# Kernel optimization log

Measured on AMD Instinct MI355X. Metric: run time of the kernel, lower is better.

## Reference

```python
import jax, jax.numpy as jnp
import numpy as np
import math

B, S, D, H = 2, 2048, 1024, 16
HD = D // H  # 64 head dim
DFF = 4 * D
ROPE_BASE = 10000.0
EPS = 1e-5


def setup_inputs() -> dict:
    key = jax.random.key(0)
    ks = jax.random.split(key, 16)
    w = lambda k, shp: jax.random.normal(k, shp, jnp.float32) * 0.02
    return {
        "x": jax.random.normal(ks[0], (B, S, D), jnp.float32),
        "Wq": w(ks[1], (D, D)), "bq": jnp.zeros((D,), jnp.float32),
        "Wk": w(ks[2], (D, D)), "bk": jnp.zeros((D,), jnp.float32),
        "Wv": w(ks[3], (D, D)), "bv": jnp.zeros((D,), jnp.float32),
        "Wo": w(ks[4], (D, D)), "bo": jnp.zeros((D,), jnp.float32),
        "W1": w(ks[5], (D, DFF)), "b1": jnp.zeros((DFF,), jnp.float32),
        "W2": w(ks[6], (DFF, D)), "b2": jnp.zeros((D,), jnp.float32),
        "g_pre": jnp.ones((D,), jnp.float32), "be_pre": jnp.zeros((D,), jnp.float32),
        "g_post": jnp.ones((D,), jnp.float32), "be_post": jnp.zeros((D,), jnp.float32),
    }


def _layernorm(x, g, b):
    mu = jnp.mean(x, axis=-1, keepdims=True)
    var = jnp.mean(jnp.square(x - mu), axis=-1, keepdims=True)
    return (x - mu) * jax.lax.rsqrt(var + EPS) * g + b


def _rope(q, k):
    # q,k: [B,H,S,HD]; standard rotary embedding on head dim
    half = HD // 2
    inv_freq = 1.0 / (ROPE_BASE ** (jnp.arange(0, HD, 2, dtype=jnp.float32) / HD))  # [half]
    pos = jnp.arange(S, dtype=jnp.float32)
    freqs = pos[:, None] * inv_freq[None, :]           # [S, half]
    emb = jnp.concatenate([freqs, freqs], axis=-1)      # [S, HD]
    cos = jnp.cos(emb)[None, None]                      # [1,1,S,HD]
    sin = jnp.sin(emb)[None, None]

    def rot_half(t):
        return jnp.concatenate([-t[..., half:], t[..., :half]], axis=-1)

    return q * cos + rot_half(q) * sin, k * cos + rot_half(k) * sin


def reference(x, Wq, bq, Wk, bk, Wv, bv, Wo, bo, W1, b1, W2, b2,
              g_pre, be_pre, g_post, be_post):
    residual = x
    xn = _layernorm(x, g_pre, be_pre)

    def split_heads(t):  # [B,S,D] -> [B,H,S,HD]
        return t.reshape(B, S, H, HD).transpose(0, 2, 1, 3)

    q = split_heads(xn @ Wq + bq)
    k = split_heads(xn @ Wk + bk)
    v = split_heads(xn @ Wv + bv)
    q, k = _rope(q, k)

    scores = jnp.einsum("bhqd,bhkd->bhqk", q, k) / math.sqrt(HD)
    attn = jax.nn.softmax(scores, axis=-1)
    # NOTE: original applies causal mask AFTER softmax with fill -1e9 (no renorm)
    causal = jnp.tril(jnp.ones((S, S), jnp.float32))
    attn = jnp.where(causal == 0, jnp.float32(-1e9), attn)

    out = jnp.einsum("bhqk,bhkd->bhqd", attn, v)        # [B,H,S,HD]
    out = out.transpose(0, 2, 1, 3).reshape(B, S, D)
    out = out @ Wo + bo
    x = residual + out

    residual = x
    xn = _layernorm(x, g_post, be_post)
    ff = jax.nn.relu(xn @ W1 + b1) @ W2 + b2
    return residual + ff
```

## Files before the change

### kernel.cpp

```cpp
#include <hip/hip_runtime.h>
#include <stdint.h>

#define B_ 2
#define S_ 2048
#define D_ 1024
#define H_ 16
#define HD_ 64
#define DFF_ 4096
#define M_ 4096
#define QKV_STR 3072

typedef float           f4_t  __attribute__((ext_vector_type(4)));
typedef unsigned int    ui4_t __attribute__((ext_vector_type(4)));
typedef unsigned int    ui2_t __attribute__((ext_vector_type(2)));
typedef unsigned short  us4_t __attribute__((ext_vector_type(4)));
typedef unsigned short  us8_t __attribute__((ext_vector_type(8)));
typedef __bf16          bf8_t __attribute__((ext_vector_type(8)));

__device__ __forceinline__ float b2f(unsigned short u) {
    union { unsigned int u; float f; } v; v.u = ((unsigned int)u) << 16; return v.f;
}
__device__ __forceinline__ unsigned short f2b(float f) {
    union { float f; unsigned int u; } v; v.f = f;
    unsigned int u = v.u + 0x7fffu + ((v.u >> 16) & 1u);
    return (unsigned short)(u >> 16);
}
__device__ __forceinline__ unsigned cvt_pk_bf16(float lo, float hi) {
    unsigned r;
    asm("v_cvt_pk_bf16_f32 %0, %1, %2" : "=v"(r) : "v"(lo), "v"(hi));
    return r;
}
__device__ __forceinline__ void gll16(const unsigned short* g, unsigned short* l) {
    __builtin_amdgcn_global_load_lds((const __attribute__((address_space(1))) unsigned int*)g,
                                     (__attribute__((address_space(3))) unsigned int*)l,
                                     16, 0, 0);
}

__global__ __launch_bounds__(256) void k_transpose(const float* __restrict__ in,
                                                   unsigned short* __restrict__ out,
                                                   int R, int C) {
    __shared__ float tile[32][33];
    const int bc = blockIdx.x * 32, br = blockIdx.y * 32;
    const int tx = threadIdx.x & 31, ty = threadIdx.x >> 5;
#pragma unroll
    for (int i = ty; i < 32; i += 8)
        tile[i][tx] = in[(size_t)(br + i) * C + bc + tx];
    __syncthreads();
#pragma unroll
    for (int i = ty; i < 32; i += 8)
        out[(size_t)(bc + i) * R + br + tx] = f2b(tile[tx][i]);
}

__global__ __launch_bounds__(256) void k_bias3(const float* __restrict__ a,
                                               const float* __restrict__ b,
                                               const float* __restrict__ c,
                                               float* __restrict__ o) {
    const int t = blockIdx.x * 256 + threadIdx.x;
    if (t < 1024) o[t] = a[t];
    else if (t < 2048) o[t] = b[t - 1024];
    else o[t] = c[t - 2048];
}

__global__ __launch_bounds__(256) void k_layernorm(const float* __restrict__ x,
                                                   const float* __restrict__ g,
                                                   const float* __restrict__ be,
                                                   unsigned short* __restrict__ out) {
    const int row = blockIdx.x;
    const int t = threadIdx.x;
    const float* xr = x + (size_t)row * D_;
    f4_t v = *(const f4_t*)&xr[t * 4];
    float s = v[0] + v[1] + v[2] + v[3];
#pragma unroll
    for (int o = 32; o >= 1; o >>= 1) s += __shfl_down(s, o);
    __shared__ float red[4];
    const int w = t >> 6, lane = t & 63;
    if (lane == 0) red[w] = s;
    __syncthreads();
    const float mean = (red[0] + red[1] + red[2] + red[3]) * (1.f / D_);
    f4_t d;
#pragma unroll
    for (int c = 0; c < 4; c++) d[c] = v[c] - mean;
    float ss = d[0]*d[0] + d[1]*d[1] + d[2]*d[2] + d[3]*d[3];
#pragma unroll
    for (int o = 32; o >= 1; o >>= 1) ss += __shfl_down(ss, o);
    __syncthreads();
    if (lane == 0) red[w] = ss;
    __syncthreads();
    const float var = (red[0] + red[1] + red[2] + red[3]) * (1.f / D_);
    const float rstd = rsqrtf(var + 1e-5f);
    f4_t gv = *(const f4_t*)&g[t * 4];
    f4_t bv = *(const f4_t*)&be[t * 4];
    us4_t o4;
#pragma unroll
    for (int c = 0; c < 4; c++) o4[c] = f2b(d[c] * rstd * gv[c] + bv[c]);
    *(us4_t*)&out[(size_t)row * D_ + t * 4] = o4;
}

#define VMW(n) asm volatile("s_waitcnt vmcnt(" #n ")" ::: "memory")
#define BAR()  __builtin_amdgcn_s_barrier()

template<int RELU, int BF16OUT, int RESID>
__global__ __launch_bounds__(256) void k_gemm_bt(const unsigned short* __restrict__ A,
                                                 const unsigned short* __restrict__ Bt,
                                                 const float* __restrict__ bias,
                                                 const float* __restrict__ resid,
                                                 void* __restrict__ Cout,
                                                 int M, int N, int K, int nbx) {
    __shared__ __align__(16) unsigned short As0[128 * 32];
    __shared__ __align__(16) unsigned short Bs0[128 * 32];
    __shared__ __align__(16) unsigned short As1[128 * 32];
    __shared__ __align__(16) unsigned short Bs1[128 * 32];
    const int tid = threadIdx.x;
    const int cpx = gridDim.x >> 3;
    const int nid = (blockIdx.x & 7) * cpx + (blockIdx.x >> 3);
    const int m0 = (nid / nbx) * 128, n0 = (nid % nbx) * 128;
    const int w = tid >> 6, lane = tid & 63;
    const int wr = w >> 1, wc = w & 1;
    const int lr = lane & 15, lg = lane >> 4;

    f4_t acc[4][4] = {};

    const int r1 = tid >> 2, q1 = tid & 3;
    const unsigned short* pA1 = A + (size_t)(m0 + r1) * K + q1 * 8;
    const unsigned short* pA2 = pA1 + (size_t)64 * K;
    const unsigned short* pB1 = Bt + (size_t)(n0 + r1) * K + q1 * 8;
    const unsigned short* pB2 = pB1 + (size_t)64 * K;
    const int wofs = w * 512;

#define STAGE(AS, BS, kk) do {                 \
        gll16(pA1 + (kk), (AS) + wofs);        \
        gll16(pA2 + (kk), (AS) + 2048 + wofs); \
        gll16(pB1 + (kk), (BS) + wofs);        \
        gll16(pB2 + (kk), (BS) + 2048 + wofs); } while (0)

#define COMPUTE(AS, BS) do {                                                     \
        bf8_t af[4], bfr[4];                                                     \
        _Pragma("unroll")                                                        \
        for (int f = 0; f < 4; f++) {                                            \
            af[f]  = *(const bf8_t*)&(AS)[(wr * 64 + f * 16 + lr) * 32 + lg * 8];\
            bfr[f] = *(const bf8_t*)&(BS)[(wc * 64 + f * 16 + lr) * 32 + lg * 8];\
        }                                                                        \
        _Pragma("unroll")                                                        \
        for (int mf = 0; mf < 4; mf++)                                           \
            _Pragma("unroll")                                                    \
            for (int nf = 0; nf < 4; nf++)                                       \
                acc[mf][nf] = __builtin_amdgcn_mfma_f32_16x16x32_bf16(           \
                    af[mf], bfr[nf], acc[mf][nf], 0, 0, 0); } while (0)

    STAGE(As0, Bs0, 0);
    for (int k0 = 0; k0 + 64 < K; k0 += 64) {
        STAGE(As1, Bs1, k0 + 32);
        VMW(4); BAR();
        COMPUTE(As0, Bs0);
        BAR();
        STAGE(As0, Bs0, k0 + 64);
        VMW(4); BAR();
        COMPUTE(As1, Bs1);
        BAR();
    }
    STAGE(As1, Bs1, K - 32);
    VMW(4); BAR();
    COMPUTE(As0, Bs0);
    VMW(0); BAR();
    COMPUTE(As1, Bs1);
#undef STAGE
#undef COMPUTE

#pragma unroll
    for (int mf = 0; mf < 4; mf++) {
#pragma unroll
        for (int nf = 0; nf < 4; nf++) {
            const int n = n0 + wc * 64 + nf * 16 + lr;
            const float bv = bias[n];
#pragma unroll
            for (int j = 0; j < 4; j++) {
                const int m = m0 + wr * 64 + mf * 16 + lg * 4 + j;
                float val = acc[mf][nf][j] + bv;
                if (RESID) val += resid[(size_t)m * N + n];
                if (RELU) val = fmaxf(val, 0.f);
                if (BF16OUT) ((unsigned short*)Cout)[(size_t)m * N + n] = f2b(val);
                else         ((float*)Cout)[(size_t)m * N + n] = val;
            }
        }
    }
}

template<int RELU, int BF16OUT, int RESID>
__global__ __launch_bounds__(256) void k_gemm64(const unsigned short* __restrict__ A,
                                                const unsigned short* __restrict__ Bt,
                                                const float* __restrict__ bias,
                                                const float* __restrict__ resid,
                                                void* __restrict__ Cout,
                                                int M, int N, int K, int nbx) {
    __shared__ __align__(16) unsigned short As0[64 * 32];
    __shared__ __align__(16) unsigned short Bs0[128 * 32];
    __shared__ __align__(16) unsigned short As1[64 * 32];
    __shared__ __align__(16) unsigned short Bs1[128 * 32];
    const int tid = threadIdx.x;
    const int cpx = gridDim.x >> 3;
    const int nid = (blockIdx.x & 7) * cpx + (blockIdx.x >> 3);
    const int m0 = (nid / nbx) * 64, n0 = (nid % nbx) * 128;
    const int w = tid >> 6, lane = tid & 63;
    const int wr = w >> 1, wc = w & 1;
    const int lr = lane & 15, lg = lane >> 4;

    f4_t acc[2][4] = {};

    const int r1 = tid >> 2, q1 = tid & 3;
    const unsigned short* pA1 = A + (size_t)(m0 + r1) * K + q1 * 8;
    const unsigned short* pB1 = Bt + (size_t)(n0 + r1) * K + q1 * 8;
    const unsigned short* pB2 = pB1 + (size_t)64 * K;
    const int wofs = w * 512;

#define STAGE(AS, BS, kk) do {                 \
        gll16(pA1 + (kk), (AS) + wofs);        \
        gll16(pB1 + (kk), (BS) + wofs);        \
        gll16(pB2 + (kk), (BS) + 2048 + wofs); } while (0)

#define COMPUTE(AS, BS) do {                                                     \
        bf8_t af[2], bfr[4];                                                     \
        _Pragma("unroll")                                                        \
        for (int f = 0; f < 2; f++)                                              \
            af[f] = *(const bf8_t*)&(AS)[(wr * 32 + f * 16 + lr) * 32 + lg * 8]; \
        _Pragma("unroll")                                                        \
        for (int f = 0; f < 4; f++)                                              \
            bfr[f] = *(const bf8_t*)&(BS)[(wc * 64 + f * 16 + lr) * 32 + lg * 8];\
        _Pragma("unroll")                                                        \
        for (int mf = 0; mf < 2; mf++)                                           \
            _Pragma("unroll")                                                    \
            for (int nf = 0; nf < 4; nf++)                                       \
                acc[mf][nf] = __builtin_amdgcn_mfma_f32_16x16x32_bf16(           \
                    af[mf], bfr[nf], acc[mf][nf], 0, 0, 0); } while (0)

    STAGE(As0, Bs0, 0);
    for (int k0 = 0; k0 + 64 < K; k0 += 64) {
        STAGE(As1, Bs1, k0 + 32);
        VMW(3); BAR();
        COMPUTE(As0, Bs0);
        BAR();
        STAGE(As0, Bs0, k0 + 64);
        VMW(3); BAR();
        COMPUTE(As1, Bs1);
        BAR();
    }
    STAGE(As1, Bs1, K - 32);
    VMW(3); BAR();
    COMPUTE(As0, Bs0);
    VMW(0); BAR();
    COMPUTE(As1, Bs1);
#undef STAGE
#undef COMPUTE

#pragma unroll
    for (int mf = 0; mf < 2; mf++) {
#pragma unroll
        for (int nf = 0; nf < 4; nf++) {
            const int n = n0 + wc * 64 + nf * 16 + lr;
            const float bv = bias[n];
#pragma unroll
            for (int j = 0; j < 4; j++) {
                const int m = m0 + wr * 32 + mf * 16 + lg * 4 + j;
                float val = acc[mf][nf][j] + bv;
                if (RESID) val += resid[(size_t)m * N + n];
                if (RELU) val = fmaxf(val, 0.f);
                if (BF16OUT) ((unsigned short*)Cout)[(size_t)m * N + n] = f2b(val);
                else         ((float*)Cout)[(size_t)m * N + n] = val;
            }
        }
    }
}

__global__ __launch_bounds__(256) void k_rope(unsigned short* __restrict__ QKV) {
    const int idx = blockIdx.x * 256 + threadIdx.x;
    const int i = idx & 31;
    const int h = (idx >> 5) & 15;
    const int s = (idx >> 9) & 2047;
    const int b = idx >> 20;
    const float freq = exp2f(-(float)i * 0.4152410118609203f);
    const float ang = (float)s * freq;
    float sn, cs;
    sincosf(ang, &sn, &cs);
    const size_t base = ((size_t)(b * S_ + s)) * QKV_STR + h * HD_ + i;
    {
        float a = b2f(QKV[base]), c2 = b2f(QKV[base + 32]);
        QKV[base]      = f2b(a * cs - c2 * sn);
        QKV[base + 32] = f2b(c2 * cs + a * sn);
    }
    {
        float a = b2f(QKV[base + 1024]), c2 = b2f(QKV[base + 1024 + 32]);
        QKV[base + 1024]      = f2b(a * cs - c2 * sn);
        QKV[base + 1024 + 32] = f2b(c2 * cs + a * sn);
    }
}

__global__ __launch_bounds__(256) void k_vchunksum(const unsigned short* __restrict__ V,
                                                   float* __restrict__ sums) {
    const int blk = blockIdx.x;
    const int bh = blk >> 5, c = blk & 31;
    const int b = bh >> 4, h = bh & 15;
    const int d = threadIdx.x & 63, r4 = threadIdx.x >> 6;
    const unsigned short* base = V + ((size_t)(b * S_ + c * 64 + r4 * 16)) * QKV_STR + h * HD_ + d;
    float s = 0.f;
#pragma unroll
    for (int r = 0; r < 16; r++) s += b2f(base[(size_t)r * QKV_STR]);
    __shared__ float red[4][64];
    red[r4][d] = s;
    __syncthreads();
    if (r4 == 0) sums[(size_t)blk * 64 + d] = red[0][d] + red[1][d] + red[2][d] + red[3][d];
}

__global__ __launch_bounds__(64) void k_vscan(const float* __restrict__ sums,
                                              float* __restrict__ pre) {
    const int bh = blockIdx.x, d = threadIdx.x;
    float cum = 0.f;
    for (int c = 0; c < 32; c++) {
        pre[((size_t)bh * 33 + c) * 64 + d] = cum;
        cum += sums[((size_t)bh * 32 + c) * 64 + d];
    }
    pre[((size_t)bh * 33 + 32) * 64 + d] = cum;
}

#define KS_STRIDE 72

__global__ __launch_bounds__(256) void k_attn_mfma(const unsigned short* __restrict__ QKV,
                                                   const float* __restrict__ vpre,
                                                   unsigned short* __restrict__ Out) {
    __shared__ __align__(16) unsigned short Ks[2][64 * KS_STRIDE];
    __shared__ __align__(16) unsigned short Vt[2][64 * 64];
    __shared__ __align__(16) unsigned short Ps[4][2][16 * KS_STRIDE];

    const int id = blockIdx.x;
    const int wg = (id & 7) * 64 + (id >> 3);
    const int qblk = 15 - (wg & 15);
    const int bh = wg >> 4;
    const int b = bh >> 4, h = bh & 15;
    const int q0 = qblk * 128;
    const int tid = threadIdx.x;
    const int wq = tid >> 6;
    const int lane = tid & 63;
    const int lr = lane & 15, lg = lane >> 4;

    const unsigned short* Qp = QKV;
    const unsigned short* Kp = QKV + 1024;
    const unsigned short* Vp = QKV + 2048;

    const int kcd = 2 * qblk + (wq >> 1);
    const int lastV = 2 * qblk + 1;
    int qb[2];
    qb[0] = (wq & 1) * 32 + lr;
    qb[1] = qb[0] + 16;

    bf8_t qfrag[2][2];
#pragma unroll
    for (int t = 0; t < 2; t++) {
        const float qs = 0.125f * 1.44269504f;
        const size_t qbase = ((size_t)(b * S_ + q0 + wq * 32 + t * 16 + lr)) * QKV_STR + h * HD_;
#pragma unroll
        for (int ks = 0; ks < 2; ks++) {
            us8_t raw = *(const us8_t*)(Qp + qbase + ks * 32 + lg * 8);
            ui4_t p;
#pragma unroll
            for (int e = 0; e < 4; e++)
                p[e] = cvt_pk_bf16(b2f(raw[e * 2]) * qs, b2f(raw[e * 2 + 1]) * qs);
            union { ui4_t u; bf8_t b; } c; c.u = p;
            qfrag[t][ks] = c.b;
        }
    }

    const int row0 = tid >> 3, g = tid & 7;
    const int row1 = row0 + 32;
    const int r7 = row0 & 7;
    const int wv = tid >> 6;
    const unsigned short* pK0 = Kp + ((size_t)(b * S_ + row0)) * QKV_STR + h * HD_ + g * 8;
    const unsigned short* pK1 = Kp + ((size_t)(b * S_ + row1)) * QKV_STR + h * HD_ + g * 8;
    const unsigned short* pV0 = Vp + ((size_t)(b * S_ + row0)) * QKV_STR + h * HD_ + g * 8;
    const unsigned short* pV1 = Vp + ((size_t)(b * S_ + row1)) * QKV_STR + h * HD_ + g * 8;
    const int sw0 = (wv ^ g) << 3;
    const int sw1 = ((wv + 4) ^ g) << 3;

    float l_run[2] = {0.f, 0.f};
    f4_t acc_o[2][4] = {};
    f4_t acc_pre[2][4] = {};

    ui4_t ck0 = *(const ui4_t*)pK0;
    ui4_t ck1 = *(const ui4_t*)pK1;
    ui4_t cv0 = *(const ui4_t*)pV0;
    ui4_t cv1 = *(const ui4_t*)pV1;
    *(ui4_t*)&Ks[0][row0 * KS_STRIDE + g * 8] = ck0;
    *(ui4_t*)&Ks[0][row1 * KS_STRIDE + g * 8] = ck1;
    {
        const unsigned short* v0 = (const unsigned short*)&cv0;
        const unsigned short* v1 = (const unsigned short*)&cv1;
#pragma unroll
        for (int e = 0; e < 8; e++) {
            const int d = g * 8 + e;
            Vt[0][d * 64 + sw0 + r7] = v0[e];
            Vt[0][d * 64 + sw1 + r7] = v1[e];
        }
    }
    {
        const size_t koff = (size_t)64 * QKV_STR;
        ck0 = *(const ui4_t*)(pK0 + koff);
        ck1 = *(const ui4_t*)(pK1 + koff);
        cv0 = *(const ui4_t*)(pV0 + koff);
        cv1 = *(const ui4_t*)(pV1 + koff);
    }
    __syncthreads();

#define VSLOT(dd, ks) ((((ks) * 4 + lg) ^ (((dd) * 2 + (lr >> 3)) & 7)) << 3)

    for (int kc = 0; kc < 32; kc++) {
        const int cur = kc & 1;
        const unsigned short* Kc = Ks[cur];
        const unsigned short* Vc = Vt[cur];

        f4_t s4[2][4] = {};
        __builtin_amdgcn_s_setprio(1);
#pragma unroll
        for (int ks = 0; ks < 2; ks++) {
#pragma unroll
            for (int kk = 0; kk < 4; kk++) {
                bf8_t kfr = *(const bf8_t*)&Kc[(kk * 16 + lr) * KS_STRIDE + ks * 32 + lg * 8];
                s4[0][kk] = __builtin_amdgcn_mfma_f32_16x16x32_bf16(kfr, qfrag[0][ks], s4[0][kk], 0, 0, 0);
                s4[1][kk] = __builtin_amdgcn_mfma_f32_16x16x32_bf16(kfr, qfrag[1][ks], s4[1][kk], 0, 0, 0);
            }
        }
        __builtin_amdgcn_s_setprio(0);

        if (kc < 31) {
            unsigned short* Kn = Ks[cur ^ 1];
            *(ui4_t*)&Kn[row0 * KS_STRIDE + g * 8] = ck0;
            *(ui4_t*)&Kn[row1 * KS_STRIDE + g * 8] = ck1;
            if (kc + 1 <= lastV) {
                unsigned short* Vn = Vt[cur ^ 1];
                const unsigned short* v0 = (const unsigned short*)&cv0;
                const unsigned short* v1 = (const unsigned short*)&cv1;
#pragma unroll
                for (int e = 0; e < 8; e++) {
                    const int d = g * 8 + e;
                    Vn[d * 64 + sw0 + r7] = v0[e];
                    Vn[d * 64 + sw1 + r7] = v1[e];
                }
            }
        }
        if (kc < 30) {
            const size_t koff = (size_t)(kc + 2) * 64 * QKV_STR;
            ck0 = *(const ui4_t*)(pK0 + koff);
            ck1 = *(const ui4_t*)(pK1 + koff);
            if (kc + 2 <= lastV) {
                cv0 = *(const ui4_t*)(pV0 + koff);
                cv1 = *(const ui4_t*)(pV1 + koff);
            }
        }

#pragma unroll
        for (int t = 0; t < 2; t++) {
            float cs = 0.f;
#pragma unroll
            for (int kk = 0; kk < 4; kk++)
#pragma unroll
                for (int j = 0; j < 4; j++) {
                    const float p = __builtin_amdgcn_exp2f(s4[t][kk][j]);
                    s4[t][kk][j] = p;
                    cs += p;
                }
            cs += __shfl_xor(cs, 16);
            cs += __shfl_xor(cs, 32);
            l_run[t] += cs;
        }

        if (kc <= kcd) {
#pragma unroll
            for (int t = 0; t < 2; t++) {
                unsigned short* Pw = Ps[wq][t];
#pragma unroll
                for (int kk = 0; kk < 4; kk++) {
                    const int kb = kk * 16 + lg * 4;
                    ui2_t wd;
                    if (kc == kcd) {
                        wd[0] = cvt_pk_bf16(kb + 0 <= qb[t] ? s4[t][kk][0] : 0.f,
                                            kb + 1 <= qb[t] ? s4[t][kk][1] : 0.f);
                        wd[1] = cvt_pk_bf16(kb + 2 <= qb[t] ? s4[t][kk][2] : 0.f,
                                            kb + 3 <= qb[t] ? s4[t][kk][3] : 0.f);
                    } else {
                        wd[0] = cvt_pk_bf16(s4[t][kk][0], s4[t][kk][1]);
                        wd[1] = cvt_pk_bf16(s4[t][kk][2], s4[t][kk][3]);
                    }
                    *(ui2_t*)&Pw[lr * KS_STRIDE + kk * 16 + lg * 4] = wd;
                }
            }
            __builtin_amdgcn_s_setprio(1);
#pragma unroll
            for (int ks = 0; ks < 2; ks++) {
                bf8_t pf0 = *(const bf8_t*)&Ps[wq][0][lr * KS_STRIDE + ks * 32 + lg * 8];
                bf8_t pf1 = *(const bf8_t*)&Ps[wq][1][lr * KS_STRIDE + ks * 32 + lg * 8];
#pragma unroll
                for (int dd = 0; dd < 4; dd++) {
                    bf8_t vf = *(const bf8_t*)&Vc[(dd * 16 + lr) * 64 + VSLOT(dd, ks)];
                    acc_o[0][dd] = __builtin_amdgcn_mfma_f32_16x16x32_bf16(vf, pf0, acc_o[0][dd], 0, 0, 0);
                    acc_o[1][dd] = __builtin_amdgcn_mfma_f32_16x16x32_bf16(vf, pf1, acc_o[1][dd], 0, 0, 0);
                }
            }
            __builtin_amdgcn_s_setprio(0);

            if (kc == kcd) {
#pragma unroll
                for (int t = 0; t < 2; t++) {
                    unsigned short* Pw = Ps[wq][t];
#pragma unroll
                    for (int kk = 0; kk < 4; kk++) {
                        const int kb = kk * 16 + lg * 4;
                        ui2_t wd;
                        wd[0] = (kb + 0 <= qb[t] ? 0x3f80u : 0u) | ((kb + 1 <= qb[t] ? 0x3f80u : 0u) << 16);
                        wd[1] = (kb + 2 <= qb[t] ? 0x3f80u : 0u) | ((kb + 3 <= qb[t] ? 0x3f80u : 0u) << 16);
                        *(ui2_t*)&Pw[lr * KS_STRIDE + kk * 16 + lg * 4] = wd;
                    }
                }
#pragma unroll
                for (int ks = 0; ks < 2; ks++) {
                    bf8_t pf0 = *(const bf8_t*)&Ps[wq][0][lr * KS_STRIDE + ks * 32 + lg * 8];
                    bf8_t pf1 = *(const bf8_t*)&Ps[wq][1][lr * KS_STRIDE + ks * 32 + lg * 8];
#pragma unroll
                    for (int dd = 0; dd < 4; dd++) {
                        bf8_t vf = *(const bf8_t*)&Vc[(dd * 16 + lr) * 64 + VSLOT(dd, ks)];
                        acc_pre[0][dd] = __builtin_amdgcn_mfma_f32_16x16x32_bf16(vf, pf0, acc_pre[0][dd], 0, 0, 0);
                        acc_pre[1][dd] = __builtin_amdgcn_mfma_f32_16x16x32_bf16(vf, pf1, acc_pre[1][dd], 0, 0, 0);
                    }
                }
            }
        }
        __syncthreads();
    }
#undef VSLOT

    const float* Cq = vpre + ((size_t)bh * 33 + kcd) * 64;
    const float* Ct = vpre + ((size_t)bh * 33 + 32) * 64;
#pragma unroll
    for (int t = 0; t < 2; t++) {
        const float inv_l = 1.f / l_run[t];
        const size_t obase = ((size_t)(b * S_ + q0 + wq * 32 + t * 16 + lr)) * D_ + h * HD_;
#pragma unroll
        for (int dd = 0; dd < 4; dd++) {
            const f4_t tq4 = *(const f4_t*)&Cq[dd * 16 + lg * 4];
            const f4_t tt4 = *(const f4_t*)&Ct[dd * 16 + lg * 4];
            float v[4];
#pragma unroll
            for (int j = 0; j < 4; j++)
                v[j] = acc_o[t][dd][j] * inv_l - 1e9f * (tt4[j] - tq4[j] - acc_pre[t][dd][j]);
            ui2_t wd;
            wd[0] = cvt_pk_bf16(v[0], v[1]);
            wd[1] = cvt_pk_bf16(v[2], v[3]);
            *(ui2_t*)&Out[obase + dd * 16 + lg * 4] = wd;
        }
    }
}

extern "C" void kernel_launch(void* const* d_in, const int* in_sizes, int n_in,
                              void* d_out, int out_size, void* d_ws, size_t ws_size,
                              hipStream_t stream) {
    const float* x     = (const float*)d_in[0];
    const float* Wq    = (const float*)d_in[1];  const float* bq = (const float*)d_in[2];
    const float* Wk    = (const float*)d_in[3];  const float* bk = (const float*)d_in[4];
    const float* Wv    = (const float*)d_in[5];  const float* bv = (const float*)d_in[6];
    const float* Wo    = (const float*)d_in[7];  const float* bo = (const float*)d_in[8];
    const float* W1    = (const float*)d_in[9];  const float* b1 = (const float*)d_in[10];
    const float* W2    = (const float*)d_in[11]; const float* b2 = (const float*)d_in[12];
    const float* gpre  = (const float*)d_in[13]; const float* bepre  = (const float*)d_in[14];
    const float* gpost = (const float*)d_in[15]; const float* bepost = (const float*)d_in[16];

    char* ws = (char*)d_ws;
    const size_t MB = 1024 * 1024;
    unsigned short* WqkvT = (unsigned short*)(ws + 0 * MB);
    unsigned short* WoT   = (unsigned short*)(ws + 6 * MB);
    unsigned short* W1T   = (unsigned short*)(ws + 8 * MB);
    unsigned short* W2T   = (unsigned short*)(ws + 16 * MB);
    unsigned short* xn    = (unsigned short*)(ws + 24 * MB);
    unsigned short* QKV   = (unsigned short*)(ws + 32 * MB);
    unsigned short* att   = (unsigned short*)(ws + 56 * MB);
    unsigned short* h1    = (unsigned short*)(ws + 24 * MB);
    unsigned short* x2n   = (unsigned short*)(ws + 56 * MB);
    float*          x2    = (float*)(ws + 64 * MB);
    float*          bqkv  = (float*)(ws + 80 * MB);
    float*          vpre  = (float*)(ws + 80 * MB + 16384);
    float*          vsum  = (float*)(ws + 81 * MB);

    k_transpose<<<dim3(32, 32),  256, 0, stream>>>(Wq, WqkvT, D_, D_);
    k_transpose<<<dim3(32, 32),  256, 0, stream>>>(Wk, WqkvT + 1024 * 1024, D_, D_);
    k_transpose<<<dim3(32, 32),  256, 0, stream>>>(Wv, WqkvT + 2048 * 1024, D_, D_);
    k_transpose<<<dim3(32, 32),  256, 0, stream>>>(Wo, WoT, D_, D_);
    k_transpose<<<dim3(128, 32), 256, 0, stream>>>(W1, W1T, D_, DFF_);
    k_transpose<<<dim3(32, 128), 256, 0, stream>>>(W2, W2T, DFF_, D_);
    k_bias3<<<12, 256, 0, stream>>>(bq, bk, bv, bqkv);

    k_layernorm<<<M_, 256, 0, stream>>>(x, gpre, bepre, xn);

    k_gemm_bt<0, 1, 0><<<768, 256, 0, stream>>>(xn, WqkvT, bqkv, nullptr, QKV, M_, QKV_STR, D_, 24);

    k_rope<<<8192, 256, 0, stream>>>(QKV);
    k_vchunksum<<<1024, 256, 0, stream>>>(QKV + 2048, vsum);
    k_vscan<<<32, 64, 0, stream>>>(vsum, vpre);

    k_attn_mfma<<<512, 256, 0, stream>>>(QKV, vpre, att);

    k_gemm64<0, 0, 1><<<512, 256, 0, stream>>>(att, WoT, bo, x, x2, M_, D_, D_, 8);

    k_layernorm<<<M_, 256, 0, stream>>>(x2, gpost, bepost, x2n);

    k_gemm_bt<1, 1, 0><<<1024, 256, 0, stream>>>(x2n, W1T, b1, nullptr, h1, M_, DFF_, D_, 32);
    k_gemm64<0, 0, 1><<<512, 256, 0, stream>>>(h1, W2T, b2, x2, (float*)d_out, M_, D_, DFF_, 8);
}
```

Baseline: 268.5 us.

## Merge prep kernels, fuse RoPE into QKV GEMM, split-K the W2 GEMM

Replaces the six weight transposes and the bias copy with one prep kernel, which also precomputes a cos/sin RoPE table. RoPE is applied in the QKV GEMM epilogue from that table, so the separate read-modify-write RoPE pass over Q and K is gone. The FF2 GEMM now uses the 128x128 tile kernel with split-K=2, writing bf16 partials that a new combine kernel sums with the bias and residual. This trades an extra partial-sum pass and bf16 rounding of the partials for more parallelism and fewer launches. Workspace buffers are also reassigned.

```diff
diff --git a/kernel.cpp b/kernel.cpp
--- a/kernel.cpp
+++ b/kernel.cpp
@@ -36,29 +36,51 @@
                                      16, 0, 0);
 }
 
-__global__ __launch_bounds__(256) void k_transpose(const float* __restrict__ in,
-                                                   unsigned short* __restrict__ out,
-                                                   int R, int C) {
-    __shared__ float tile[32][33];
-    const int bc = blockIdx.x * 32, br = blockIdx.y * 32;
-    const int tx = threadIdx.x & 31, ty = threadIdx.x >> 5;
-#pragma unroll
-    for (int i = ty; i < 32; i += 8)
-        tile[i][tx] = in[(size_t)(br + i) * C + bc + tx];
-    __syncthreads();
-#pragma unroll
-    for (int i = ty; i < 32; i += 8)
-        out[(size_t)(bc + i) * R + br + tx] = f2b(tile[tx][i]);
-}
-
-__global__ __launch_bounds__(256) void k_bias3(const float* __restrict__ a,
-                                               const float* __restrict__ b,
-                                               const float* __restrict__ c,
-                                               float* __restrict__ o) {
-    const int t = blockIdx.x * 256 + threadIdx.x;
-    if (t < 1024) o[t] = a[t];
-    else if (t < 2048) o[t] = b[t - 1024];
-    else o[t] = c[t - 2048];
+__global__ __launch_bounds__(256) void k_prep(const float* __restrict__ Wq, const float* __restrict__ Wk,
+                                              const float* __restrict__ Wv, const float* __restrict__ Wo,
+                                              const float* __restrict__ W1, const float* __restrict__ W2,
+                                              const float* __restrict__ bq, const float* __restrict__ bk,
+                                              const float* __restrict__ bv,
+                                              unsigned short* __restrict__ WqkvT, unsigned short* __restrict__ WoT,
+                                              unsigned short* __restrict__ W1T, unsigned short* __restrict__ W2T,
+                                              float* __restrict__ bqkv, float* __restrict__ tab) {
+    const int j = blockIdx.x;
+    if (j < 12288) {
+        const float* src; unsigned short* dst; int R, C, jj;
+        if (j < 3072)      { const int r = j >> 10; src = r == 0 ? Wq : (r == 1 ? Wk : Wv);
+                             dst = WqkvT + (size_t)r * 1024 * 1024; R = 1024; C = 1024; jj = j & 1023; }
+        else if (j < 4096) { src = Wo; dst = WoT; R = 1024; C = 1024; jj = j - 3072; }
+        else if (j < 8192) { src = W1; dst = W1T; R = 1024; C = 4096; jj = j - 4096; }
+        else               { src = W2; dst = W2T; R = 4096; C = 1024; jj = j - 8192; }
+        const int ntx = C >> 5;
+        const int bc = (jj % ntx) * 32, br = (jj / ntx) * 32;
+        __shared__ float tile[32][33];
+        const int tx = threadIdx.x & 31, ty = threadIdx.x >> 5;
+#pragma unroll
+        for (int i = ty; i < 32; i += 8)
+            tile[i][tx] = src[(size_t)(br + i) * C + bc + tx];
+        __syncthreads();
+#pragma unroll
+        for (int i = ty; i < 32; i += 8)
+            dst[(size_t)(bc + i) * R + br + tx] = f2b(tile[tx][i]);
+    } else if (j < 12300) {
+        const int t = (j - 12288) * 256 + threadIdx.x;
+        if (t < 1024) bqkv[t] = bq[t];
+        else if (t < 2048) bqkv[t] = bk[t - 1024];
+        else if (t < 3072) bqkv[t] = bv[t - 2048];
+    } else {
+        const int base = (j - 12300) * 256 + threadIdx.x;
+#pragma unroll
+        for (int e = 0; e < 32; e++) {
+            const int idx = base + e * 2048;
+            const int s = idx >> 5, i = idx & 31;
+            const float freq = exp2f(-(float)i * 0.4152410118609203f);
+            float sn, cs;
+            sincosf((float)s * freq, &sn, &cs);
+            tab[s * 64 + i] = cs;
+            tab[s * 64 + 32 + i] = sn;
+        }
+    }
 }
 
 __global__ __launch_bounds__(256) void k_layernorm(const float* __restrict__ x,
@@ -99,20 +121,23 @@
 #define VMW(n) asm volatile("s_waitcnt vmcnt(" #n ")" ::: "memory")
 #define BAR()  __builtin_amdgcn_s_barrier()
 
-template<int RELU, int BF16OUT, int RESID>
+template<int RELU, int BF16OUT, int RESID, int ROPE, int SPLIT>
 __global__ __launch_bounds__(256) void k_gemm_bt(const unsigned short* __restrict__ A,
                                                  const unsigned short* __restrict__ Bt,
                                                  const float* __restrict__ bias,
                                                  const float* __restrict__ resid,
                                                  void* __restrict__ Cout,
-                                                 int M, int N, int K, int nbx) {
+                                                 const float* __restrict__ tab,
+                                                 int M, int N, int K, int ldk, int nbx) {
     __shared__ __align__(16) unsigned short As0[128 * 32];
     __shared__ __align__(16) unsigned short Bs0[128 * 32];
     __shared__ __align__(16) unsigned short As1[128 * 32];
     __shared__ __align__(16) unsigned short Bs1[128 * 32];
     const int tid = threadIdx.x;
     const int cpx = gridDim.x >> 3;
-    const int nid = (blockIdx.x & 7) * cpx + (blockIdx.x >> 3);
+    int nid = (blockIdx.x & 7) * cpx + (blockIdx.x >> 3);
+    int half = 0;
+    if (SPLIT) { half = nid >> 8; nid &= 255; A += 2048 * half; Bt += 2048 * half; }
     const int m0 = (nid / nbx) * 128, n0 = (nid % nbx) * 128;
     const int w = tid >> 6, lane = tid & 63;
     const int wr = w >> 1, wc = w & 1;
@@ -121,10 +146,10 @@
     f4_t acc[4][4] = {};
 
     const int r1 = tid >> 2, q1 = tid & 3;
-    const unsigned short* pA1 = A + (size_t)(m0 + r1) * K + q1 * 8;
-    const unsigned short* pA2 = pA1 + (size_t)64 * K;
-    const unsigned short* pB1 = Bt + (size_t)(n0 + r1) * K + q1 * 8;
-    const unsigned short* pB2 = pB1 + (size_t)64 * K;
+    const unsigned short* pA1 = A + (size_t)(m0 + r1) * ldk + q1 * 8;
+    const unsigned short* pA2 = pA1 + (size_t)64 * ldk;
+    const unsigned short* pB1 = Bt + (size_t)(n0 + r1) * ldk + q1 * 8;
+    const unsigned short* pB2 = pB1 + (size_t)64 * ldk;
     const int wofs = w * 512;
 
 #define STAGE(AS, BS, kk) do {                 \
@@ -166,6 +191,61 @@
 #undef STAGE
 #undef COMPUTE
 
+    if (SPLIT) {
+        unsigned short* outp = (unsigned short*)Cout + (size_t)half * ((size_t)M * N);
+#pragma unroll
+        for (int mf = 0; mf < 4; mf++)
+#pragma unroll
+            for (int nf = 0; nf < 4; nf++) {
+                const int n = n0 + wc * 64 + nf * 16 + lr;
+#pragma unroll
+                for (int j = 0; j < 4; j++) {
+                    const int m = m0 + wr * 64 + mf * 16 + lg * 4 + j;
+                    outp[(size_t)m * N + n] = f2b(acc[mf][nf][j]);
+                }
+            }
+        return;
+    }
+    if (ROPE) {
+#pragma unroll
+        for (int mf = 0; mf < 4; mf++)
+#pragma unroll
+            for (int nf = 0; nf < 4; nf++) {
+                const float bv = bias[n0 + wc * 64 + nf * 16 + lr];
+#pragma unroll
+                for (int j = 0; j < 4; j++) acc[mf][nf][j] += bv;
+            }
+        if (n0 < 2048) {
+#pragma unroll
+            for (int mf = 0; mf < 4; mf++)
+#pragma unroll
+                for (int j = 0; j < 4; j++) {
+                    const int srow = (m0 + wr * 64 + mf * 16 + lg * 4 + j) & 2047;
+                    const float* tr = tab + srow * 64;
+#pragma unroll
+                    for (int t = 0; t < 2; t++) {
+                        const float cs = tr[t * 16 + lr];
+                        const float sn = tr[32 + t * 16 + lr];
+                        const float lo = acc[mf][t][j], hi = acc[mf][t + 2][j];
+                        acc[mf][t][j]     = lo * cs - hi * sn;
+                        acc[mf][t + 2][j] = hi * cs + lo * sn;
+                    }
+                }
+        }
+        unsigned short* outp = (unsigned short*)Cout;
+#pragma unroll
+        for (int mf = 0; mf < 4; mf++)
+#pragma unroll
+            for (int nf = 0; nf < 4; nf++) {
+                const int n = n0 + wc * 64 + nf * 16 + lr;
+#pragma unroll
+                for (int j = 0; j < 4; j++) {
+                    const int m = m0 + wr * 64 + mf * 16 + lg * 4 + j;
+                    outp[(size_t)m * N + n] = f2b(acc[mf][nf][j]);
+                }
+            }
+        return;
+    }
 #pragma unroll
     for (int mf = 0; mf < 4; mf++) {
 #pragma unroll
@@ -191,7 +271,7 @@
                                                 const float* __restrict__ bias,
                                                 const float* __restrict__ resid,
                                                 void* __restrict__ Cout,
-                                                int M, int N, int K, int nbx) {
+                                                int M, int N, int K, int ldk, int nbx) {
     __shared__ __align__(16) unsigned short As0[64 * 32];
     __shared__ __align__(16) unsigned short Bs0[128 * 32];
     __shared__ __align__(16) unsigned short As1[64 * 32];
@@ -207,9 +287,9 @@
     f4_t acc[2][4] = {};
 
     const int r1 = tid >> 2, q1 = tid & 3;
-    const unsigned short* pA1 = A + (size_t)(m0 + r1) * K + q1 * 8;
-    const unsigned short* pB1 = Bt + (size_t)(n0 + r1) * K + q1 * 8;
-    const unsigned short* pB2 = pB1 + (size_t)64 * K;
+    const unsigned short* pA1 = A + (size_t)(m0 + r1) * ldk + q1 * 8;
+    const unsigned short* pB1 = Bt + (size_t)(n0 + r1) * ldk + q1 * 8;
+    const unsigned short* pB2 = pB1 + (size_t)64 * ldk;
     const int wofs = w * 512;
 
 #define STAGE(AS, BS, kk) do {                 \
@@ -270,27 +350,24 @@
     }
 }
 
-__global__ __launch_bounds__(256) void k_rope(unsigned short* __restrict__ QKV) {
-    const int idx = blockIdx.x * 256 + threadIdx.x;
-    const int i = idx & 31;
-    const int h = (idx >> 5) & 15;
-    const int s = (idx >> 9) & 2047;
-    const int b = idx >> 20;
-    const float freq = exp2f(-(float)i * 0.4152410118609203f);
-    const float ang = (float)s * freq;
-    float sn, cs;
-    sincosf(ang, &sn, &cs);
-    const size_t base = ((size_t)(b * S_ + s)) * QKV_STR + h * HD_ + i;
-    {
-        float a = b2f(QKV[base]), c2 = b2f(QKV[base + 32]);
-        QKV[base]      = f2b(a * cs - c2 * sn);
-        QKV[base + 32] = f2b(c2 * cs + a * sn);
-    }
-    {
-        float a = b2f(QKV[base + 1024]), c2 = b2f(QKV[base + 1024 + 32]);
-        QKV[base + 1024]      = f2b(a * cs - c2 * sn);
-        QKV[base + 1024 + 32] = f2b(c2 * cs + a * sn);
-    }
+__global__ __launch_bounds__(256) void k_comb(const unsigned short* __restrict__ p,
+                                              const float* __restrict__ x2,
+                                              const float* __restrict__ b2,
+                                              float* __restrict__ out) {
+    const size_t idx = ((size_t)blockIdx.x * 256 + threadIdx.x) * 8;
+    us8_t a = *(const us8_t*)(p + idx);
+    us8_t b = *(const us8_t*)(p + (size_t)M_ * D_ + idx);
+    const int n = (int)(idx & (D_ - 1));
+    f4_t x0 = *(const f4_t*)(x2 + idx), x1 = *(const f4_t*)(x2 + idx + 4);
+    f4_t b0 = *(const f4_t*)(b2 + n),  b1 = *(const f4_t*)(b2 + n + 4);
+    f4_t o0, o1;
+#pragma unroll
+    for (int c = 0; c < 4; c++) {
+        o0[c] = x0[c] + b0[c] + b2f(a[c]) + b2f(b[c]);
+        o1[c] = x1[c] + b1[c] + b2f(a[4 + c]) + b2f(b[4 + c]);
+    }
+    *(f4_t*)(out + idx) = o0;
+    *(f4_t*)(out + idx + 4) = o1;
 }
 
 __global__ __launch_bounds__(256) void k_vchunksum(const unsigned short* __restrict__ V,
@@ -570,42 +647,43 @@
 
     char* ws = (char*)d_ws;
     const size_t MB = 1024 * 1024;
+    unsigned short* psplit = (unsigned short*)(ws + 0 * MB);
     unsigned short* WqkvT = (unsigned short*)(ws + 0 * MB);
     unsigned short* WoT   = (unsigned short*)(ws + 6 * MB);
     unsigned short* W1T   = (unsigned short*)(ws + 8 * MB);
     unsigned short* W2T   = (unsigned short*)(ws + 16 * MB);
     unsigned short* xn    = (unsigned short*)(ws + 24 * MB);
+    unsigned short* x2n   = (unsigned short*)(ws + 24 * MB);
     unsigned short* QKV   = (unsigned short*)(ws + 32 * MB);
+    unsigned short* h1    = (unsigned short*)(ws + 32 * MB);
     unsigned short* att   = (unsigned short*)(ws + 56 * MB);
-    unsigned short* h1    = (unsigned short*)(ws + 24 * MB);
-    unsigned short* x2n   = (unsigned short*)(ws + 56 * MB);
     float*          x2    = (float*)(ws + 64 * MB);
     float*          bqkv  = (float*)(ws + 80 * MB);
     float*          vpre  = (float*)(ws + 80 * MB + 16384);
+    float*          tab   = (float*)(ws + 80 * MB + 512 * 1024);
     float*          vsum  = (float*)(ws + 81 * MB);
 
-    k_transpose<<<dim3(32, 32),  256, 0, stream>>>(Wq, WqkvT, D_, D_);
-    k_transpose<<<dim3(32, 32),  256, 0, stream>>>(Wk, WqkvT + 1024 * 1024, D_, D_);
-    k_transpose<<<dim3(32, 32),  256, 0, stream>>>(Wv, WqkvT + 2048 * 1024, D_, D_);
-    k_transpose<<<dim3(32, 32),  256, 0, stream>>>(Wo, WoT, D_, D_);
-    k_transpose<<<dim3(128, 32), 256, 0, stream>>>(W1, W1T, D_, DFF_);
-    k_transpose<<<dim3(32, 128), 256, 0, stream>>>(W2, W2T, DFF_, D_);
-    k_bias3<<<12, 256, 0, stream>>>(bq, bk, bv, bqkv);
+    k_prep<<<12308, 256, 0, stream>>>(Wq, Wk, Wv, Wo, W1, W2, bq, bk, bv,
+                                      WqkvT, WoT, W1T, W2T, bqkv, tab);
 
     k_layernorm<<<M_, 256, 0, stream>>>(x, gpre, bepre, xn);
 
-    k_gemm_bt<0, 1, 0><<<768, 256, 0, stream>>>(xn, WqkvT, bqkv, nullptr, QKV, M_, QKV_STR, D_, 24);
-
-    k_rope<<<8192, 256, 0, stream>>>(QKV);
+    k_gemm_bt<0, 1, 0, 1, 0><<<768, 256, 0, stream>>>(xn, WqkvT, bqkv, nullptr, QKV, tab,
+                                                      M_, QKV_STR, D_, D_, 24);
+
     k_vchunksum<<<1024, 256, 0, stream>>>(QKV + 2048, vsum);
     k_vscan<<<32, 64, 0, stream>>>(vsum, vpre);
 
     k_attn_mfma<<<512, 256, 0, stream>>>(QKV, vpre, att);
 
-    k_gemm64<0, 0, 1><<<512, 256, 0, stream>>>(att, WoT, bo, x, x2, M_, D_, D_, 8);
+    k_gemm64<0, 0, 1><<<512, 256, 0, stream>>>(att, WoT, bo, x, x2, M_, D_, D_, D_, 8);
 
     k_layernorm<<<M_, 256, 0, stream>>>(x2, gpost, bepost, x2n);
 
-    k_gemm_bt<1, 1, 0><<<1024, 256, 0, stream>>>(x2n, W1T, b1, nullptr, h1, M_, DFF_, D_, 32);
-    k_gemm64<0, 0, 1><<<512, 256, 0, stream>>>(h1, W2T, b2, x2, (float*)d_out, M_, D_, DFF_, 8);
-}
+    k_gemm_bt<1, 1, 0, 0, 0><<<1024, 256, 0, stream>>>(x2n, W1T, b1, nullptr, h1, nullptr,
+                                                       M_, DFF_, D_, D_, 32);
+
+    k_gemm_bt<0, 1, 0, 0, 1><<<512, 256, 0, stream>>>(h1, W2T, nullptr, nullptr, psplit, nullptr,
+                                                      M_, D_, 2048, DFF_, 8);
+    k_comb<<<2048, 256, 0, stream>>>(psplit, x2, b2, (float*)d_out);
+}
```

After: 249.7 us, median of 2. 1.08x faster.
